# Performance work log

Hardware: AMD Instinct MI355X
Metric: run time of the kernel (lower is better)

Reference implementation:

```python
import jax, jax.numpy as jnp
import numpy as np

D_MODEL = 528
N_HEADS = 16
FEAT = 16           # feature_dim
HEAD_DIM = 33       # d_model // num_heads == 2*FEAT + 1 (required by the module's math)
WINDOW = 64
EPS = 1e-9


def setup_inputs() -> dict:
    key = jax.random.key(0)
    ks = jax.random.split(key, 10)
    B, S = 2, 2048
    hidden_states = jax.random.normal(ks[0], (B, S, D_MODEL), dtype=jnp.float32)
    attention_mask = jnp.ones((B, S), dtype=jnp.int32)
    sc = 0.02
    # weights stored as (in, out); torch Linear applies x @ W.T so this is the transposed weight
    Wq_lin = jax.random.normal(ks[1], (D_MODEL, FEAT * N_HEADS), dtype=jnp.float32) * sc
    Wk_lin = jax.random.normal(ks[2], (D_MODEL, FEAT * N_HEADS), dtype=jnp.float32) * sc
    Wv_lin = jax.random.normal(ks[3], (D_MODEL, HEAD_DIM * N_HEADS), dtype=jnp.float32) * sc
    Wo_lin = jax.random.normal(ks[4], (HEAD_DIM * N_HEADS, D_MODEL), dtype=jnp.float32) * sc
    Wq_win = jax.random.normal(ks[5], (D_MODEL, D_MODEL), dtype=jnp.float32) * sc
    Wk_win = jax.random.normal(ks[6], (D_MODEL, D_MODEL), dtype=jnp.float32) * sc
    Wv_win = jax.random.normal(ks[7], (D_MODEL, D_MODEL), dtype=jnp.float32) * sc
    Wo_win = jax.random.normal(ks[8], (D_MODEL, D_MODEL), dtype=jnp.float32) * sc
    return {
        "hidden_states": hidden_states,
        "attention_mask": attention_mask,
        "Wq_lin": Wq_lin, "Wk_lin": Wk_lin, "Wv_lin": Wv_lin, "Wo_lin": Wo_lin,
        "Wq_win": Wq_win, "Wk_win": Wk_win, "Wv_win": Wv_win, "Wo_win": Wo_win,
    }


def _linear_attention(x, mask, Wq, Wk, Wv, Wo):
    B, S, _ = x.shape
    q = (x @ Wq).reshape(B, S, N_HEADS, FEAT).transpose(0, 2, 1, 3)      # bhsf
    k = (x @ Wk).reshape(B, S, N_HEADS, FEAT).transpose(0, 2, 1, 3)
    v = (x @ Wv).reshape(B, S, N_HEADS, HEAD_DIM).transpose(0, 2, 1, 3)  # bhse
    # Taylor feature map: [1, q, 0.5*q^2] -> feature dim 2*FEAT+1 == HEAD_DIM
    qe = jnp.concatenate([jnp.ones_like(q[..., :1]), q, 0.5 * q * q], axis=-1)
    ke = jnp.concatenate([jnp.ones_like(k[..., :1]), k, 0.5 * k * k], axis=-1)
    kv = jnp.einsum('bhnd,bhne->bhde', ke, v)          # (B,H,Dexp,HEAD_DIM)
    qkv = jnp.einsum('bhnd,bhde->bhne', qe, kv)        # (B,H,S,HEAD_DIM)
    # z[b,h,n,e] = (sum_d qe[b,h,n,d]) * ksum[b,h,e]  (faithful to torch einsum with size-1 n)
    z = qe.sum(-1, keepdims=True) * ke.sum(2, keepdims=True)  # (B,H,S,Dexp==HEAD_DIM)
    out = qkv / (z + EPS)
    out = jnp.where((mask == 0)[:, None, :, None], 0.0, out)
    out = out.transpose(0, 2, 1, 3).reshape(B, S, N_HEADS * HEAD_DIM)
    return out @ Wo


def _window_attention(x, mask, Wq, Wk, Wv, Wo):
    B, S, _ = x.shape
    q = (x @ Wq).reshape(B, S, N_HEADS, HEAD_DIM).transpose(0, 2, 1, 3)
    k = (x @ Wk).reshape(B, S, N_HEADS, HEAD_DIM).transpose(0, 2, 1, 3)
    v = (x @ Wv).reshape(B, S, N_HEADS, HEAD_DIM).transpose(0, 2, 1, 3)
    scores = jnp.einsum('bhnd,bhmd->bhnm', q, k) / np.sqrt(HEAD_DIM).astype(np.float32)
    # tril(diagonal=window_size-1): allow key index m <= n + WINDOW - 1
    i = jnp.arange(S)[:, None]
    j = jnp.arange(S)[None, :]
    band = (j <= i + WINDOW - 1)
    neg_inf = jnp.asarray(-jnp.inf, scores.dtype)
    scores = jnp.where(band[None, None], scores, neg_inf)
    scores = jnp.where((mask == 0)[:, None, None, :], neg_inf, scores)
    attn = jax.nn.softmax(scores, axis=-1)
    out = jnp.einsum('bhnm,bhmd->bhnd', attn, v)
    out = out.transpose(0, 2, 1, 3).reshape(B, S, D_MODEL)
    return out @ Wo


def reference(hidden_states, attention_mask,
              Wq_lin, Wk_lin, Wv_lin, Wo_lin,
              Wq_win, Wk_win, Wv_win, Wo_win):
    lin = _linear_attention(hidden_states, attention_mask, Wq_lin, Wk_lin, Wv_lin, Wo_lin)
    win = _window_attention(hidden_states, attention_mask, Wq_win, Wk_win, Wv_win, Wo_win)
    return lin + win
```

## Files before the change

kernel.cpp:

```cpp
#include <hip/hip_runtime.h>

#define NH 16
#define FEAT 16
#define HD 33
#define DM 528
#define WIN 64
#define EPSF 1e-9f
#define K1C (0.17407765595569785f * 1.4426950408889634f)
#define KP 544
#define KSPLIT 1632
#define NPROJ 2112
#define KOUT 1056
#define OPS 4352
#define NCH 16
#define ZPARTS 4

typedef float f32x4 __attribute__((ext_vector_type(4)));
typedef short short8 __attribute__((ext_vector_type(8)));

__device__ inline ushort f2bf(float f) {
  uint u = __float_as_uint(f);
  uint r = u + 0x7fffu + ((u >> 16) & 1u);
  return (ushort)(r >> 16);
}
__device__ inline ushort f2bf_tr(float f) { return (ushort)(__float_as_uint(f) >> 16); }
__device__ inline float bf2f(ushort u) { return __uint_as_float(((uint)u) << 16); }

__global__ __launch_bounds__(256) void prep_all(const float* __restrict__ x,
                                                const float* __restrict__ Wq_lin,
                                                const float* __restrict__ Wk_lin,
                                                const float* __restrict__ Wv_lin,
                                                const float* __restrict__ Wo_lin,
                                                const float* __restrict__ Wq_win,
                                                const float* __restrict__ Wk_win,
                                                const float* __restrict__ Wv_win,
                                                const float* __restrict__ Wo_win,
                                                ushort* __restrict__ xhi,
                                                ushort* __restrict__ xlo,
                                                ushort* __restrict__ Wqks,
                                                ushort* __restrict__ WprojT,
                                                ushort* __restrict__ WoT2, int M) {
  const int stride = gridDim.x * 256;
  const int tid0 = blockIdx.x * 256 + threadIdx.x;
  for (int j = tid0; j < M * 68; j += stride) {
    int row = j / 68, c8 = (j - row * 68) * 8;
    short8 h8, l8;
    if (c8 < DM) {
      float4 f0 = *(const float4*)&x[(size_t)row * DM + c8];
      float4 f1 = *(const float4*)&x[(size_t)row * DM + c8 + 4];
      float vv[8] = {f0.x, f0.y, f0.z, f0.w, f1.x, f1.y, f1.z, f1.w};
#pragma unroll
      for (int z = 0; z < 8; ++z) {
        ushort h = f2bf(vv[z]);
        h8[z] = (short)h;
        l8[z] = (short)f2bf(vv[z] - bf2f(h));
      }
    } else {
      h8 = (short8){0, 0, 0, 0, 0, 0, 0, 0};
      l8 = h8;
    }
    *(short8*)&xhi[(size_t)row * KP + c8] = h8;
    *(short8*)&xlo[(size_t)row * KP + c8] = l8;
  }
  for (int i = tid0; i < 512 * KSPLIT; i += stride) {
    int n = i / KSPLIT, kp = i - n * KSPLIT;
    int seg = kp / KP, kk = kp - seg * KP;
    float v = 0.f;
    if (kk < DM) v = (n < 256) ? Wq_lin[(size_t)kk * 256 + n] : Wk_lin[(size_t)kk * 256 + (n - 256)];
    ushort h = f2bf(v);
    if (seg == 2) h = f2bf(v - bf2f(h));
    Wqks[i] = h;
  }
  for (int i = tid0; i < NPROJ * KP; i += stride) {
    int n = i / KP, k = i - n * KP;
    float v = 0.f;
    if (k < DM) {
      if (n < DM) v = Wq_win[(size_t)k * DM + n];
      else if (n < 2 * DM) v = Wk_win[(size_t)k * DM + (n - DM)] * K1C;
      else if (n < 3 * DM) v = Wv_win[(size_t)k * DM + (n - 2 * DM)];
      else v = Wv_lin[(size_t)k * DM + (n - 3 * DM)];
    }
    WprojT[i] = f2bf(v);
  }
  for (int i = tid0; i < DM * KOUT; i += stride) {
    int n = i / KOUT, k = i - n * KOUT;
    float v = (k < DM) ? Wo_lin[(size_t)k * DM + n] : Wo_win[(size_t)(k - DM) * DM + n];
    WoT2[i] = f2bf(v);
  }
}

__global__ __launch_bounds__(256) void proj_fused(const ushort* __restrict__ xhi,
                                                  const ushort* __restrict__ xlo,
                                                  const ushort* __restrict__ Wqks,
                                                  const ushort* __restrict__ WprojT,
                                                  float* __restrict__ qk,
                                                  ushort* __restrict__ qkvw,
                                                  float* __restrict__ v_lin,
                                                  const int* __restrict__ maskp,
                                                  int S) {
  __shared__ ushort As[128][36];
  __shared__ ushort Bs[128][36];
  const int bm = blockIdx.x * 128;
  const int tid = threadIdx.x;
  const int lane = tid & 63, w = tid >> 6;
  const int lo = lane & 15, hi = lane >> 4;
  const int wr = w >> 1, wc = w & 1;
  const short8 zv = {0, 0, 0, 0, 0, 0, 0, 0};
  f32x4 acc[4][4];
#pragma unroll
  for (int mb = 0; mb < 4; ++mb)
#pragma unroll
    for (int nb = 0; nb < 4; ++nb) acc[mb][nb] = (f32x4){0.f, 0.f, 0.f, 0.f};

  if (blockIdx.y < 17) {
    const int bn = blockIdx.y * 128;
    for (int k0 = 0; k0 < KP; k0 += 32) {
      short8 a_ld[2], b_ld[2];
#pragma unroll
      for (int p = 0; p < 2; ++p) {
        int c = tid + p * 256;
        int row = c >> 2, cc = c & 3;
        a_ld[p] = *(const short8*)&xhi[(size_t)(bm + row) * KP + k0 + cc * 8];
        int bnr = bn + row;
        b_ld[p] = (bnr < NPROJ) ? *(const short8*)&WprojT[(size_t)bnr * KP + k0 + cc * 8] : zv;
      }
      __syncthreads();
#pragma unroll
      for (int p = 0; p < 2; ++p) {
        int c = tid + p * 256;
        int row = c >> 2, cc = c & 3;
        *(short8*)&As[row][cc * 8] = a_ld[p];
        *(short8*)&Bs[row][cc * 8] = b_ld[p];
      }
      __syncthreads();
      short8 afr[4], bfr[4];
#pragma unroll
      for (int mb = 0; mb < 4; ++mb) afr[mb] = *(const short8*)&As[wr * 64 + 16 * mb + lo][8 * hi];
#pragma unroll
      for (int nb = 0; nb < 4; ++nb) bfr[nb] = *(const short8*)&Bs[wc * 64 + 16 * nb + lo][8 * hi];
#pragma unroll
      for (int mb = 0; mb < 4; ++mb)
#pragma unroll
        for (int nb = 0; nb < 4; ++nb)
          acc[mb][nb] = __builtin_amdgcn_mfma_f32_16x16x32_bf16(afr[mb], bfr[nb], acc[mb][nb], 0, 0, 0);
    }
#pragma unroll
    for (int nb = 0; nb < 4; ++nb) {
      const int col = bn + wc * 64 + 16 * nb + lo;
      if (col >= NPROJ) continue;
      const int seg = col / DM;
      const int cc = col - seg * DM;
      if (seg == 3) {
#pragma unroll
        for (int mb = 0; mb < 4; ++mb)
#pragma unroll
          for (int r = 0; r < 4; ++r) {
            int row = bm + wr * 64 + 16 * mb + 4 * hi + r;
            v_lin[(size_t)row * DM + cc] = acc[mb][nb][r];
          }
      } else {
        const uint h = ((uint)cc * 993u) >> 15;
        const int e = cc - (int)h * 33;
        ushort* dst = qkvw + (size_t)seg * (32u * (uint)S * 40u);
#pragma unroll
        for (int mb = 0; mb < 4; ++mb)
#pragma unroll
          for (int r = 0; r < 4; ++r) {
            int row = bm + wr * 64 + 16 * mb + 4 * hi + r;
            int b = (row >= S) ? 1 : 0;
            int nn = row - b * S;
            float val = acc[mb][nb][r];
            if (seg == 2) {
              size_t tb = (size_t)(b * NH + (int)h) * 40;
              dst[(tb + e) * S + nn] = f2bf(val);
              if (e == 0) {
                dst[(tb + 33) * S + nn] = 0x3F80;
#pragma unroll
                for (int z = 34; z < 40; ++z) dst[(tb + z) * S + nn] = 0;
              }
            } else {
              size_t base = ((size_t)(b * NH + (int)h) * S + nn) * 40;
              dst[base + e] = f2bf(val);
              if (e == 0) {
                ushort pad33 = (seg == 0) ? (ushort)0x3F80
                                          : (maskp[row] ? (ushort)0 : f2bf(-1e30f));
                dst[base + 33] = pad33;
#pragma unroll
                for (int z = 34; z < 40; ++z) dst[base + z] = 0;
              }
            }
          }
      }
    }
  } else {
    const int bn = (blockIdx.y - 17) * 128;
    for (int k0 = 0; k0 < KSPLIT; k0 += 32) {
      const int seg = k0 / KP;
      const int kk = k0 - seg * KP;
      const ushort* xsrc = (seg == 1) ? xlo : xhi;
      short8 a_ld[2], b_ld[2];
#pragma unroll
      for (int p = 0; p < 2; ++p) {
        int c = tid + p * 256;
        int row = c >> 2, cc = c & 3;
        a_ld[p] = *(const short8*)&xsrc[(size_t)(bm + row) * KP + kk + cc * 8];
        b_ld[p] = *(const short8*)&Wqks[(size_t)(bn + row) * KSPLIT + k0 + cc * 8];
      }
      __syncthreads();
#pragma unroll
      for (int p = 0; p < 2; ++p) {
        int c = tid + p * 256;
        int row = c >> 2, cc = c & 3;
        *(short8*)&As[row][cc * 8] = a_ld[p];
        *(short8*)&Bs[row][cc * 8] = b_ld[p];
      }
      __syncthreads();
      short8 afr[4], bfr[4];
#pragma unroll
      for (int mb = 0; mb < 4; ++mb) afr[mb] = *(const short8*)&As[wr * 64 + 16 * mb + lo][8 * hi];
#pragma unroll
      for (int nb = 0; nb < 4; ++nb) bfr[nb] = *(const short8*)&Bs[wc * 64 + 16 * nb + lo][8 * hi];
#pragma unroll
      for (int mb = 0; mb < 4; ++mb)
#pragma unroll
        for (int nb = 0; nb < 4; ++nb)
          acc[mb][nb] = __builtin_amdgcn_mfma_f32_16x16x32_bf16(afr[mb], bfr[nb], acc[mb][nb], 0, 0, 0);
    }
#pragma unroll
    for (int mb = 0; mb < 4; ++mb)
#pragma unroll
      for (int nb = 0; nb < 4; ++nb) {
        int col = bn + wc * 64 + 16 * nb + lo;
#pragma unroll
        for (int r = 0; r < 4; ++r) {
          int row = bm + wr * 64 + 16 * mb + 4 * hi + r;
          qk[(size_t)row * 512 + col] = acc[mb][nb][r];
        }
      }
  }
}

__global__ __launch_bounds__(256) void gemm_out(const ushort* __restrict__ A,
                                                const ushort* __restrict__ Bt,
                                                float* __restrict__ C, int S) {
  __shared__ ushort As[128][36];
  __shared__ ushort Bs[128][36];
  const int bm = blockIdx.x * 128, bn = blockIdx.y * 128;
  const int tid = threadIdx.x;
  const int lane = tid & 63, w = tid >> 6;
  const int lo = lane & 15, hi = lane >> 4;
  const int wr = w >> 1, wc = w & 1;
  f32x4 acc[4][4];
#pragma unroll
  for (int mb = 0; mb < 4; ++mb)
#pragma unroll
    for (int nb = 0; nb < 4; ++nb) acc[mb][nb] = (f32x4){0.f, 0.f, 0.f, 0.f};
  const short8 zv = {0, 0, 0, 0, 0, 0, 0, 0};

  for (int k0 = 0; k0 < KOUT; k0 += 32) {
    short8 a_ld[2], b_ld[2];
#pragma unroll
    for (int p = 0; p < 2; ++p) {
      int c = tid + p * 256;
      int row = c >> 2, cc = c & 3;
      a_ld[p] = *(const short8*)&A[(size_t)(bm + row) * KOUT + k0 + cc * 8];
      int bnr = bn + row;
      b_ld[p] = (bnr < DM) ? *(const short8*)&Bt[(size_t)bnr * KOUT + k0 + cc * 8] : zv;
    }
    __syncthreads();
#pragma unroll
    for (int p = 0; p < 2; ++p) {
      int c = tid + p * 256;
      int row = c >> 2, cc = c & 3;
      *(short8*)&As[row][cc * 8] = a_ld[p];
      *(short8*)&Bs[row][cc * 8] = b_ld[p];
    }
    __syncthreads();
    short8 afr[4], bfr[4];
#pragma unroll
    for (int mb = 0; mb < 4; ++mb) afr[mb] = *(const short8*)&As[wr * 64 + 16 * mb + lo][8 * hi];
#pragma unroll
    for (int nb = 0; nb < 4; ++nb) bfr[nb] = *(const short8*)&Bs[wc * 64 + 16 * nb + lo][8 * hi];
#pragma unroll
    for (int mb = 0; mb < 4; ++mb)
#pragma unroll
      for (int nb = 0; nb < 4; ++nb)
        acc[mb][nb] = __builtin_amdgcn_mfma_f32_16x16x32_bf16(afr[mb], bfr[nb], acc[mb][nb], 0, 0, 0);
  }
#pragma unroll
  for (int nb = 0; nb < 4; ++nb) {
    const int col = bn + wc * 64 + 16 * nb + lo;
    if (col >= DM) continue;
#pragma unroll
    for (int mb = 0; mb < 4; ++mb)
#pragma unroll
      for (int r = 0; r < 4; ++r) {
        int row = bm + wr * 64 + 16 * mb + 4 * hi + r;
        C[(size_t)row * DM + col] = acc[mb][nb][r];
      }
  }
}

__global__ __launch_bounds__(256) void lin_red(const float* __restrict__ kvp,
                                               float* __restrict__ kvr) {
  int bh = blockIdx.x;
  for (int i = threadIdx.x; i < 1188; i += 256) {
    float s = 0.f;
#pragma unroll
    for (int c = 0; c < NCH; ++c) s += kvp[(size_t)(bh * NCH + c) * 1188 + i];
    kvr[(size_t)bh * 1188 + i] = s;
  }
}

__global__ __launch_bounds__(256) void win_kv(const ushort* __restrict__ qwb,
                                              const ushort* __restrict__ kwb,
                                              const ushort* __restrict__ vwbT,
                                              ushort* __restrict__ Opart,
                                              const float* __restrict__ qk,
                                              const float* __restrict__ v_lin,
                                              float* __restrict__ kvp,
                                              int B, int S, int NT2) {
  __shared__ ushort sh[4][32][72];
  const int tid = threadIdx.x;
  const int NWINBLK = NT2 * 32 * ZPARTS;
  const int bx = blockIdx.x;

  if (bx < NWINBLK) {
    const int bh = bx & 31;
    const int qp = bx >> 5;
    const int part = qp / NT2;
    const int qt = NT2 - 1 - (qp - part * NT2);
    const int NT = NT2 * 2;
    const int T = min(NT, 2 * qt + 3);
    if (part >= T) return;
    const int n0 = qt * 128;
    const int lane = tid & 63, w = tid >> 6;
    const int lo = lane & 15, hi = lane >> 4;
    const short8 zv = {0, 0, 0, 0, 0, 0, 0, 0};
    ushort (*Ps)[32][72] = sh;

    short8 qf[2][2];
#pragma unroll
    for (int qr = 0; qr < 2; ++qr) {
      const ushort* qrow = qwb + ((size_t)bh * S + n0 + w * 32 + qr * 16 + lo) * 40;
      qf[qr][0] = *(const short8*)&qrow[8 * hi];
      qf[qr][1] = (hi == 0) ? *(const short8*)&qrow[32] : zv;
    }

    const ushort* kb = kwb + (size_t)bh * S * 40;
    const ushort* vb = vwbT + (size_t)bh * 40 * S;
    int evc[3];
#pragma unroll
    for (int eb = 0; eb < 3; ++eb) {
      int e = 16 * eb + lo;
      evc[eb] = (e > 39) ? 39 : e;
    }

    f32x4 Oacc[2][3];
#pragma unroll
    for (int qr = 0; qr < 2; ++qr)
#pragma unroll
      for (int eb = 0; eb < 3; ++eb) Oacc[qr][eb] = (f32x4){0.f, 0.f, 0.f, 0.f};

    for (int t = part; t < T; t += ZPARTS) {
      const int m0 = t * 64;
      short8 kf0[4], kf1[4];
#pragma unroll
      for (int bb = 0; bb < 4; ++bb) {
        const ushort* kr = kb + (size_t)(m0 + 16 * bb + lo) * 40;
        kf0[bb] = *(const short8*)&kr[8 * hi];
        kf1[bb] = *(const short8*)&kr[32];
      }
      short8 vf0[3], vf1[3];
#pragma unroll
      for (int eb = 0; eb < 3; ++eb) {
        const ushort* vr = vb + (size_t)evc[eb] * S + m0;
        vf0[eb] = *(const short8*)&vr[8 * hi];
        vf1[eb] = *(const short8*)&vr[32 + 8 * hi];
      }

      f32x4 accS[2][4];
#pragma unroll
      for (int qr = 0; qr < 2; ++qr)
#pragma unroll
        for (int bb = 0; bb < 4; ++bb) accS[qr][bb] = (f32x4){0.f, 0.f, 0.f, 0.f};
      __builtin_amdgcn_s_setprio(1);
#pragma unroll
      for (int bb = 0; bb < 4; ++bb)
#pragma unroll
        for (int qr = 0; qr < 2; ++qr) {
          accS[qr][bb] = __builtin_amdgcn_mfma_f32_16x16x32_bf16(qf[qr][0], kf0[bb], accS[qr][bb], 0, 0, 0);
          accS[qr][bb] = __builtin_amdgcn_mfma_f32_16x16x32_bf16(qf[qr][1], kf1[bb], accS[qr][bb], 0, 0, 0);
        }
      __builtin_amdgcn_s_setprio(0);

      const bool boundary = (m0 > n0);
      const int dmn = m0 - n0;
#pragma unroll
      for (int qr = 0; qr < 2; ++qr)
#pragma unroll
        for (int bb = 0; bb < 4; ++bb)
#pragma unroll
          for (int r = 0; r < 4; ++r) {
            float p = exp2f(accS[qr][bb][r]);
            if (boundary) {
              int rr = w * 32 + qr * 16 + 4 * hi + r;
              int c = 16 * bb + lo;
              if (c > rr + 63 - dmn) p = 0.f;
            }
            Ps[w][qr * 16 + 4 * hi + r][16 * bb + lo] = f2bf_tr(p);
          }

      __builtin_amdgcn_s_setprio(1);
#pragma unroll
      for (int qr = 0; qr < 2; ++qr) {
        short8 pf0 = *(const short8*)&Ps[w][qr * 16 + lo][8 * hi];
        short8 pf1 = *(const short8*)&Ps[w][qr * 16 + lo][32 + 8 * hi];
#pragma unroll
        for (int eb = 0; eb < 3; ++eb) {
          Oacc[qr][eb] = __builtin_amdgcn_mfma_f32_16x16x32_bf16(pf0, vf0[eb], Oacc[qr][eb], 0, 0, 0);
          Oacc[qr][eb] = __builtin_amdgcn_mfma_f32_16x16x32_bf16(pf1, vf1[eb], Oacc[qr][eb], 0, 0, 0);
        }
      }
      __builtin_amdgcn_s_setprio(0);
    }

    const size_t ob = ((size_t)(bh * NT2 + qt) * ZPARTS + part) * OPS;
#pragma unroll
    for (int qr = 0; qr < 2; ++qr)
#pragma unroll
      for (int eb = 0; eb < 3; ++eb) {
        int e = 16 * eb + lo;
        if (e < 34) {
#pragma unroll
          for (int r = 0; r < 4; ++r)
            Opart[ob + (size_t)(w * 32 + qr * 16 + 4 * hi + r) * 34 + e] = f2bf(Oacc[qr][eb][r]);
        }
      }
  } else {
    const int idx = bx - NWINBLK;
    const int bh = idx & 31, chunk = idx >> 5;
    const int b = bh >> 4, h = bh & 15;
    float* kraw = (float*)sh;
    float* vsh = kraw + 64 * 17;
    if (tid < 64) { vsh[tid * 36 + 33] = 1.f; vsh[tid * 36 + 34] = 0.f; vsh[tid * 36 + 35] = 0.f; }
    f32x4 acc0 = {0.f, 0.f, 0.f, 0.f}, acc1 = {0.f, 0.f, 0.f, 0.f};
    const int d0 = tid / 9, c40 = (tid % 9) * 4;
    const int idx1 = tid + 256;
    const int d1 = idx1 / 9, c41 = (idx1 % 9) * 4;
    const int SC = S / NCH;
    const int nbeg = chunk * SC;
    __syncthreads();
    for (int n0 = nbeg; n0 < nbeg + SC; n0 += 64) {
      {
        int row = tid >> 2, f4 = (tid & 3) * 4;
        float4 kv4 = *(const float4*)&qk[(size_t)(b * S + n0 + row) * 512 + 256 + h * 16 + f4];
        kraw[row * 17 + f4 + 0] = kv4.x; kraw[row * 17 + f4 + 1] = kv4.y;
        kraw[row * 17 + f4 + 2] = kv4.z; kraw[row * 17 + f4 + 3] = kv4.w;
      }
      for (int i = tid; i < 64 * 33; i += 256) {
        int n = i / 33, e = i - n * 33;
        vsh[n * 36 + e] = v_lin[(size_t)(b * S + n0 + n) * DM + h * HD + e];
      }
      __syncthreads();
#pragma unroll 4
      for (int n = 0; n < 64; ++n) {
        {
          float ke;
          if (d0 == 0) ke = 1.f;
          else if (d0 < 17) ke = kraw[n * 17 + d0 - 1];
          else { float kk = kraw[n * 17 + d0 - 17]; ke = 0.5f * kk * kk; }
          f32x4 v = *(const f32x4*)&vsh[n * 36 + c40];
          acc0 += ke * v;
        }
        if (idx1 < 297) {
          float ke;
          if (d1 < 17) ke = kraw[n * 17 + d1 - 1];
          else { float kk = kraw[n * 17 + d1 - 17]; ke = 0.5f * kk * kk; }
          f32x4 v = *(const f32x4*)&vsh[n * 36 + c41];
          acc1 += ke * v;
        }
      }
      __syncthreads();
    }
    float* dst = kvp + (size_t)(bh * NCH + chunk) * 1188;
    *(f32x4*)&dst[d0 * 36 + c40] = acc0;
    if (idx1 < 297) *(f32x4*)&dst[d1 * 36 + c41] = acc1;
  }
}

__global__ __launch_bounds__(256) void comb_lin(const ushort* __restrict__ Opart,
                                                const float* __restrict__ qk,
                                                const float* __restrict__ kvr,
                                                const int* __restrict__ mask,
                                                ushort* __restrict__ cat,
                                                int B, int S, int NT2) {
  __shared__ float shf[160];
  const int tid = threadIdx.x;
  const int NCOMB = NT2 * 32;
  const int bx = blockIdx.x;

  if (bx < NCOMB) {
    const int bh = bx & 31;
    const int qt = bx >> 5;
    const int b = bh >> 4, h = bh & 15;
    const int T = min(NT2 * 2, 2 * qt + 3);
    const int P = min(ZPARTS, T);
    const size_t base = (size_t)(bh * NT2 + qt) * ZPARTS * OPS;
    float* linv = shf;
    if (tid < 128) {
      float l = 0.f;
      for (int p = 0; p < P; ++p) l += bf2f(Opart[base + (size_t)p * OPS + tid * 34 + 33]);
      linv[tid] = (l > 0.f) ? 1.f / l : 0.f;
    }
    __syncthreads();
    for (int i = tid; i < 128 * 33; i += 256) {
      int row = i / 33, e = i - row * 33;
      float o = 0.f;
      for (int p = 0; p < P; ++p) o += bf2f(Opart[base + (size_t)p * OPS + row * 34 + e]);
      int n = qt * 128 + row;
      cat[((size_t)(b * S + n)) * KOUT + DM + h * HD + e] = f2bf(o * linv[row]);
    }
  } else {
    const int bs = bx - NCOMB;
    const int b = (bs >= S) ? 1 : 0;
    float* qsh = shf;
    __shared__ float qsh2[NH * 17];
    qsh = qsh2;
    for (int i = tid; i < NH * FEAT; i += 256)
      qsh[(i >> 4) * 17 + (i & 15)] = qk[(size_t)bs * 512 + i];
    __syncthreads();
    const int msk = mask[bs];
    for (int o = tid; o < DM; o += 256) {
      uint h = ((uint)o * 993u) >> 15;
      int e = o - (int)h * 33;
      const float* kvh = kvr + (size_t)(b * NH + (int)h) * 1188;
      float qsum = 1.f, qkv = kvh[e];
#pragma unroll
      for (int f = 0; f < FEAT; ++f) {
        float q = qsh[h * 17 + f];
        float q2 = 0.5f * q * q;
        qsum += q + q2;
        qkv += q * kvh[(1 + f) * 36 + e] + q2 * kvh[(17 + f) * 36 + e];
      }
      float z = qsum * kvh[e * 36 + 33];
      float outv = qkv / (z + EPSF);
      if (msk == 0) outv = 0.f;
      cat[(size_t)bs * KOUT + o] = f2bf(outv);
    }
  }
}

extern "C" void kernel_launch(void* const* d_in, const int* in_sizes, int n_in,
                              void* d_out, int out_size, void* d_ws, size_t ws_size,
                              hipStream_t stream) {
  const float* x      = (const float*)d_in[0];
  const int*   mask   = (const int*)d_in[1];
  const float* Wq_lin = (const float*)d_in[2];
  const float* Wk_lin = (const float*)d_in[3];
  const float* Wv_lin = (const float*)d_in[4];
  const float* Wo_lin = (const float*)d_in[5];
  const float* Wq_win = (const float*)d_in[6];
  const float* Wk_win = (const float*)d_in[7];
  const float* Wv_win = (const float*)d_in[8];
  const float* Wo_win = (const float*)d_in[9];
  float* out = (float*)d_out;

  const int BS = in_sizes[1];
  const int B = 2;
  const int S = BS / B;
  const int NT2 = S / 128;
  const int M = BS;

  float* ws = (float*)d_ws;
  float* qk      = ws;  ws += (size_t)BS * 512;
  float* v_lin   = ws;  ws += (size_t)BS * DM;
  float* kvp     = ws;  ws += (size_t)B * NH * NCH * 1188;
  float* kvr     = ws;  ws += (size_t)B * NH * 1188;
  ushort* ub     = (ushort*)ws;
  ushort* x_hi   = ub;  ub += (size_t)M * KP;
  ushort* x_lo   = ub;  ub += (size_t)M * KP;
  ushort* qkvw   = ub;  ub += (size_t)3 * 32 * S * 40;
  ushort* cat    = ub;  ub += (size_t)M * KOUT;
  ushort* WprojT = ub;  ub += (size_t)NPROJ * KP;
  ushort* WoT2   = ub;  ub += (size_t)DM * KOUT;
  ushort* Wqks   = ub;  ub += (size_t)512 * KSPLIT;
  ushort* Opart  = ub;  ub += (size_t)32 * NT2 * ZPARTS * OPS;

  ushort* qwb  = qkvw;
  ushort* kwb  = qkvw + (size_t)32 * S * 40;
  ushort* vwbT = qkvw + (size_t)64 * S * 40;

  dim3 blk(256);

  prep_all<<<2048, blk, 0, stream>>>(x, Wq_lin, Wk_lin, Wv_lin, Wo_lin,
                                     Wq_win, Wk_win, Wv_win, Wo_win,
                                     x_hi, x_lo, Wqks, WprojT, WoT2, M);

  proj_fused<<<dim3(M / 128, 21), blk, 0, stream>>>(x_hi, x_lo, Wqks, WprojT,
                                                    qk, qkvw, v_lin, mask, S);

  win_kv<<<dim3(NT2 * 32 * ZPARTS + B * NH * NCH), blk, 0, stream>>>(
      qwb, kwb, vwbT, Opart, qk, v_lin, kvp, B, S, NT2);

  lin_red<<<dim3(B * NH), blk, 0, stream>>>(kvp, kvr);

  comb_lin<<<dim3(NT2 * 32 + BS), blk, 0, stream>>>(Opart, qk, kvr, mask, cat, B, S, NT2);

  gemm_out<<<dim3(M / 128, (DM + 127) / 128), blk, 0, stream>>>(cat, WoT2, out, S);
}
```

Before: 193.1 us.

## Split-K the qk projection with atomics, persistent work queue, smaller gemm_out tiles

The qk projection's three-segment K loop is split across separate blocks that accumulate into a zeroed qk buffer with atomicAdd, which raises the block count. win_kv becomes a persistent kernel that pulls window and linear-kv work items from eight atomic counters, replacing the fixed grid mapping. gemm_out moves to 64-row tiles so more blocks run. The changes trade extra atomic traffic, a qk zeroing pass and queue overhead for better load balance and occupancy, and atomic accumulation makes the summation order nondeterministic.

```diff
diff --git a/kernel.cpp b/kernel.cpp
--- a/kernel.cpp
+++ b/kernel.cpp
@@ -39,9 +39,12 @@
                                                 ushort* __restrict__ xlo,
                                                 ushort* __restrict__ Wqks,
                                                 ushort* __restrict__ WprojT,
-                                                ushort* __restrict__ WoT2, int M) {
+                                                ushort* __restrict__ WoT2,
+                                                float* __restrict__ qk,
+                                                int* __restrict__ ctr, int M) {
   const int stride = gridDim.x * 256;
   const int tid0 = blockIdx.x * 256 + threadIdx.x;
+  if (tid0 < 8) ctr[tid0] = 0;
   for (int j = tid0; j < M * 68; j += stride) {
     int row = j / 68, c8 = (j - row * 68) * 8;
     short8 h8, l8;
@@ -62,6 +65,8 @@
     *(short8*)&xhi[(size_t)row * KP + c8] = h8;
     *(short8*)&xlo[(size_t)row * KP + c8] = l8;
   }
+  for (int i = tid0; i < M * 128; i += stride)
+    ((float4*)qk)[i] = make_float4(0.f, 0.f, 0.f, 0.f);
   for (int i = tid0; i < 512 * KSPLIT; i += stride) {
     int n = i / KSPLIT, kp = i - n * KSPLIT;
     int seg = kp / KP, kk = kp - seg * KP;
@@ -193,18 +198,19 @@
       }
     }
   } else {
-    const int bn = (blockIdx.y - 17) * 128;
-    for (int k0 = 0; k0 < KSPLIT; k0 += 32) {
-      const int seg = k0 / KP;
-      const int kk = k0 - seg * KP;
-      const ushort* xsrc = (seg == 1) ? xlo : xhi;
+    const int yy = blockIdx.y - 17;
+    const int seg = yy >> 2;
+    const int bn = (yy & 3) * 128;
+    const ushort* xsrc = (seg == 1) ? xlo : xhi;
+    const int kb = seg * KP;
+    for (int k0 = 0; k0 < KP; k0 += 32) {
       short8 a_ld[2], b_ld[2];
 #pragma unroll
       for (int p = 0; p < 2; ++p) {
         int c = tid + p * 256;
         int row = c >> 2, cc = c & 3;
-        a_ld[p] = *(const short8*)&xsrc[(size_t)(bm + row) * KP + kk + cc * 8];
-        b_ld[p] = *(const short8*)&Wqks[(size_t)(bn + row) * KSPLIT + k0 + cc * 8];
+        a_ld[p] = *(const short8*)&xsrc[(size_t)(bm + row) * KP + k0 + cc * 8];
+        b_ld[p] = *(const short8*)&Wqks[(size_t)(bn + row) * KSPLIT + kb + k0 + cc * 8];
       }
       __syncthreads();
 #pragma unroll
@@ -234,7 +240,7 @@
 #pragma unroll
         for (int r = 0; r < 4; ++r) {
           int row = bm + wr * 64 + 16 * mb + 4 * hi + r;
-          qk[(size_t)row * 512 + col] = acc[mb][nb][r];
+          atomicAdd(&qk[(size_t)row * 512 + col], acc[mb][nb][r]);
         }
       }
   }
@@ -243,46 +249,52 @@
 __global__ __launch_bounds__(256) void gemm_out(const ushort* __restrict__ A,
                                                 const ushort* __restrict__ Bt,
                                                 float* __restrict__ C, int S) {
-  __shared__ ushort As[128][36];
+  __shared__ ushort As[64][36];
   __shared__ ushort Bs[128][36];
-  const int bm = blockIdx.x * 128, bn = blockIdx.y * 128;
+  const int bm = blockIdx.x * 64, bn = blockIdx.y * 128;
   const int tid = threadIdx.x;
   const int lane = tid & 63, w = tid >> 6;
   const int lo = lane & 15, hi = lane >> 4;
-  const int wr = w >> 1, wc = w & 1;
-  f32x4 acc[4][4];
-#pragma unroll
-  for (int mb = 0; mb < 4; ++mb)
+  const int wr = w & 1, wc = w >> 1;
+  f32x4 acc[2][4];
+#pragma unroll
+  for (int mb = 0; mb < 2; ++mb)
 #pragma unroll
     for (int nb = 0; nb < 4; ++nb) acc[mb][nb] = (f32x4){0.f, 0.f, 0.f, 0.f};
   const short8 zv = {0, 0, 0, 0, 0, 0, 0, 0};
 
   for (int k0 = 0; k0 < KOUT; k0 += 32) {
-    short8 a_ld[2], b_ld[2];
+    short8 a_ld, b_ld[2];
+    {
+      int row = tid >> 2, cc = tid & 3;
+      a_ld = *(const short8*)&A[(size_t)(bm + row) * KOUT + k0 + cc * 8];
+    }
 #pragma unroll
     for (int p = 0; p < 2; ++p) {
       int c = tid + p * 256;
       int row = c >> 2, cc = c & 3;
-      a_ld[p] = *(const short8*)&A[(size_t)(bm + row) * KOUT + k0 + cc * 8];
       int bnr = bn + row;
       b_ld[p] = (bnr < DM) ? *(const short8*)&Bt[(size_t)bnr * KOUT + k0 + cc * 8] : zv;
     }
     __syncthreads();
+    {
+      int row = tid >> 2, cc = tid & 3;
+      *(short8*)&As[row][cc * 8] = a_ld;
+    }
 #pragma unroll
     for (int p = 0; p < 2; ++p) {
       int c = tid + p * 256;
       int row = c >> 2, cc = c & 3;
-      *(short8*)&As[row][cc * 8] = a_ld[p];
       *(short8*)&Bs[row][cc * 8] = b_ld[p];
     }
     __syncthreads();
-    short8 afr[4], bfr[4];
-#pragma unroll
-    for (int mb = 0; mb < 4; ++mb) afr[mb] = *(const short8*)&As[wr * 64 + 16 * mb + lo][8 * hi];
+    short8 afr[2], bfr[4];
+#pragma unroll
+    for (int mb = 0; mb < 2; ++mb) afr[mb] = *(const short8*)&As[wr * 32 + 16 * mb + lo][8 * hi];
 #pragma unroll
     for (int nb = 0; nb < 4; ++nb) bfr[nb] = *(const short8*)&Bs[wc * 64 + 16 * nb + lo][8 * hi];
 #pragma unroll
-    for (int mb = 0; mb < 4; ++mb)
+    for (int mb = 0; mb < 2; ++mb)
 #pragma unroll
       for (int nb = 0; nb < 4; ++nb)
         acc[mb][nb] = __builtin_amdgcn_mfma_f32_16x16x32_bf16(afr[mb], bfr[nb], acc[mb][nb], 0, 0, 0);
@@ -292,10 +304,10 @@
     const int col = bn + wc * 64 + 16 * nb + lo;
     if (col >= DM) continue;
 #pragma unroll
-    for (int mb = 0; mb < 4; ++mb)
+    for (int mb = 0; mb < 2; ++mb)
 #pragma unroll
       for (int r = 0; r < 4; ++r) {
-        int row = bm + wr * 64 + 16 * mb + 4 * hi + r;
+        int row = bm + wr * 32 + 16 * mb + 4 * hi + r;
         C[(size_t)row * DM + col] = acc[mb][nb][r];
       }
   }
@@ -319,173 +331,195 @@
                                               const float* __restrict__ qk,
                                               const float* __restrict__ v_lin,
                                               float* __restrict__ kvp,
+                                              int* __restrict__ ctr,
                                               int B, int S, int NT2) {
   __shared__ ushort sh[4][32][72];
+  __shared__ int s_item;
   const int tid = threadIdx.x;
-  const int NWINBLK = NT2 * 32 * ZPARTS;
-  const int bx = blockIdx.x;
-
-  if (bx < NWINBLK) {
-    const int bh = bx & 31;
-    const int qp = bx >> 5;
-    const int part = qp / NT2;
-    const int qt = NT2 - 1 - (qp - part * NT2);
-    const int NT = NT2 * 2;
-    const int T = min(NT, 2 * qt + 3);
-    if (part >= T) return;
-    const int n0 = qt * 128;
-    const int lane = tid & 63, w = tid >> 6;
-    const int lo = lane & 15, hi = lane >> 4;
-    const short8 zv = {0, 0, 0, 0, 0, 0, 0, 0};
-    ushort (*Ps)[32][72] = sh;
-
-    short8 qf[2][2];
-#pragma unroll
-    for (int qr = 0; qr < 2; ++qr) {
-      const ushort* qrow = qwb + ((size_t)bh * S + n0 + w * 32 + qr * 16 + lo) * 40;
-      qf[qr][0] = *(const short8*)&qrow[8 * hi];
-      qf[qr][1] = (hi == 0) ? *(const short8*)&qrow[32] : zv;
-    }
-
-    const ushort* kb = kwb + (size_t)bh * S * 40;
-    const ushort* vb = vwbT + (size_t)bh * 40 * S;
-    int evc[3];
-#pragma unroll
-    for (int eb = 0; eb < 3; ++eb) {
-      int e = 16 * eb + lo;
-      evc[eb] = (e > 39) ? 39 : e;
-    }
-
-    f32x4 Oacc[2][3];
-#pragma unroll
-    for (int qr = 0; qr < 2; ++qr)
-#pragma unroll
-      for (int eb = 0; eb < 3; ++eb) Oacc[qr][eb] = (f32x4){0.f, 0.f, 0.f, 0.f};
-
-    for (int t = part; t < T; t += ZPARTS) {
-      const int m0 = t * 64;
-      short8 kf0[4], kf1[4];
-#pragma unroll
-      for (int bb = 0; bb < 4; ++bb) {
-        const ushort* kr = kb + (size_t)(m0 + 16 * bb + lo) * 40;
-        kf0[bb] = *(const short8*)&kr[8 * hi];
-        kf1[bb] = *(const short8*)&kr[32];
-      }
-      short8 vf0[3], vf1[3];
-#pragma unroll
-      for (int eb = 0; eb < 3; ++eb) {
-        const ushort* vr = vb + (size_t)evc[eb] * S + m0;
-        vf0[eb] = *(const short8*)&vr[8 * hi];
-        vf1[eb] = *(const short8*)&vr[32 + 8 * hi];
-      }
-
-      f32x4 accS[2][4];
-#pragma unroll
-      for (int qr = 0; qr < 2; ++qr)
-#pragma unroll
-        for (int bb = 0; bb < 4; ++bb) accS[qr][bb] = (f32x4){0.f, 0.f, 0.f, 0.f};
-      __builtin_amdgcn_s_setprio(1);
-#pragma unroll
-      for (int bb = 0; bb < 4; ++bb)
-#pragma unroll
-        for (int qr = 0; qr < 2; ++qr) {
-          accS[qr][bb] = __builtin_amdgcn_mfma_f32_16x16x32_bf16(qf[qr][0], kf0[bb], accS[qr][bb], 0, 0, 0);
-          accS[qr][bb] = __builtin_amdgcn_mfma_f32_16x16x32_bf16(qf[qr][1], kf1[bb], accS[qr][bb], 0, 0, 0);
-        }
-      __builtin_amdgcn_s_setprio(0);
-
-      const bool boundary = (m0 > n0);
-      const int dmn = m0 - n0;
-#pragma unroll
-      for (int qr = 0; qr < 2; ++qr)
-#pragma unroll
-        for (int bb = 0; bb < 4; ++bb)
-#pragma unroll
-          for (int r = 0; r < 4; ++r) {
-            float p = exp2f(accS[qr][bb][r]);
-            if (boundary) {
-              int rr = w * 32 + qr * 16 + 4 * hi + r;
-              int c = 16 * bb + lo;
-              if (c > rr + 63 - dmn) p = 0.f;
-            }
-            Ps[w][qr * 16 + 4 * hi + r][16 * bb + lo] = f2bf_tr(p);
-          }
-
-      __builtin_amdgcn_s_setprio(1);
+  const int qid = blockIdx.x & 7;
+  const int WINQ = NT2 * 16;
+  const int QTOT = WINQ + 4 * NCH;
+
+  for (;;) {
+    __syncthreads();
+    if (tid == 0) {
+      int item = -1;
+      for (int a = 0; a < 8; ++a) {
+        int q = (qid + a) & 7;
+        int wi = atomicAdd(&ctr[q], 1);
+        if (wi < QTOT) { item = q * QTOT + wi; break; }
+      }
+      s_item = item;
+    }
+    __syncthreads();
+    const int it = s_item;
+    if (it < 0) return;
+    const int q = it / QTOT;
+    const int wi = it - q * QTOT;
+
+    if (wi < WINQ) {
+      const int qt = NT2 - 1 - (wi >> 4);
+      const int sub = wi & 15;
+      const int part = sub >> 2;
+      const int bh = q + 8 * (sub & 3);
+      const int NT = NT2 * 2;
+      const int T = min(NT, 2 * qt + 3);
+      if (part >= T) continue;
+      const int n0 = qt * 128;
+      const int lane = tid & 63, w = tid >> 6;
+      const int lo = lane & 15, hi = lane >> 4;
+      const short8 zv = {0, 0, 0, 0, 0, 0, 0, 0};
+      ushort (*Ps)[32][72] = sh;
+
+      short8 qf[2][2];
 #pragma unroll
       for (int qr = 0; qr < 2; ++qr) {
-        short8 pf0 = *(const short8*)&Ps[w][qr * 16 + lo][8 * hi];
-        short8 pf1 = *(const short8*)&Ps[w][qr * 16 + lo][32 + 8 * hi];
-#pragma unroll
-        for (int eb = 0; eb < 3; ++eb) {
-          Oacc[qr][eb] = __builtin_amdgcn_mfma_f32_16x16x32_bf16(pf0, vf0[eb], Oacc[qr][eb], 0, 0, 0);
-          Oacc[qr][eb] = __builtin_amdgcn_mfma_f32_16x16x32_bf16(pf1, vf1[eb], Oacc[qr][eb], 0, 0, 0);
-        }
-      }
-      __builtin_amdgcn_s_setprio(0);
-    }
-
-    const size_t ob = ((size_t)(bh * NT2 + qt) * ZPARTS + part) * OPS;
-#pragma unroll
-    for (int qr = 0; qr < 2; ++qr)
+        const ushort* qrow = qwb + ((size_t)bh * S + n0 + w * 32 + qr * 16 + lo) * 40;
+        qf[qr][0] = *(const short8*)&qrow[8 * hi];
+        qf[qr][1] = (hi == 0) ? *(const short8*)&qrow[32] : zv;
+      }
+
+      const ushort* kb = kwb + (size_t)bh * S * 40;
+      const ushort* vb = vwbT + (size_t)bh * 40 * S;
+      int evc[3];
 #pragma unroll
       for (int eb = 0; eb < 3; ++eb) {
         int e = 16 * eb + lo;
-        if (e < 34) {
-#pragma unroll
-          for (int r = 0; r < 4; ++r)
-            Opart[ob + (size_t)(w * 32 + qr * 16 + 4 * hi + r) * 34 + e] = f2bf(Oacc[qr][eb][r]);
-        }
-      }
-  } else {
-    const int idx = bx - NWINBLK;
-    const int bh = idx & 31, chunk = idx >> 5;
-    const int b = bh >> 4, h = bh & 15;
-    float* kraw = (float*)sh;
-    float* vsh = kraw + 64 * 17;
-    if (tid < 64) { vsh[tid * 36 + 33] = 1.f; vsh[tid * 36 + 34] = 0.f; vsh[tid * 36 + 35] = 0.f; }
-    f32x4 acc0 = {0.f, 0.f, 0.f, 0.f}, acc1 = {0.f, 0.f, 0.f, 0.f};
-    const int d0 = tid / 9, c40 = (tid % 9) * 4;
-    const int idx1 = tid + 256;
-    const int d1 = idx1 / 9, c41 = (idx1 % 9) * 4;
-    const int SC = S / NCH;
-    const int nbeg = chunk * SC;
-    __syncthreads();
-    for (int n0 = nbeg; n0 < nbeg + SC; n0 += 64) {
-      {
-        int row = tid >> 2, f4 = (tid & 3) * 4;
-        float4 kv4 = *(const float4*)&qk[(size_t)(b * S + n0 + row) * 512 + 256 + h * 16 + f4];
-        kraw[row * 17 + f4 + 0] = kv4.x; kraw[row * 17 + f4 + 1] = kv4.y;
-        kraw[row * 17 + f4 + 2] = kv4.z; kraw[row * 17 + f4 + 3] = kv4.w;
-      }
-      for (int i = tid; i < 64 * 33; i += 256) {
-        int n = i / 33, e = i - n * 33;
-        vsh[n * 36 + e] = v_lin[(size_t)(b * S + n0 + n) * DM + h * HD + e];
-      }
+        evc[eb] = (e > 39) ? 39 : e;
+      }
+
+      f32x4 Oacc[2][3];
+#pragma unroll
+      for (int qr = 0; qr < 2; ++qr)
+#pragma unroll
+        for (int eb = 0; eb < 3; ++eb) Oacc[qr][eb] = (f32x4){0.f, 0.f, 0.f, 0.f};
+
+      for (int t = part; t < T; t += ZPARTS) {
+        const int m0 = t * 64;
+        short8 kf0[4], kf1[4];
+#pragma unroll
+        for (int bb = 0; bb < 4; ++bb) {
+          const ushort* kr = kb + (size_t)(m0 + 16 * bb + lo) * 40;
+          kf0[bb] = *(const short8*)&kr[8 * hi];
+          kf1[bb] = *(const short8*)&kr[32];
+        }
+        short8 vf0[3], vf1[3];
+#pragma unroll
+        for (int eb = 0; eb < 3; ++eb) {
+          const ushort* vr = vb + (size_t)evc[eb] * S + m0;
+          vf0[eb] = *(const short8*)&vr[8 * hi];
+          vf1[eb] = *(const short8*)&vr[32 + 8 * hi];
+        }
+
+        f32x4 accS[2][4];
+#pragma unroll
+        for (int qr = 0; qr < 2; ++qr)
+#pragma unroll
+          for (int bb = 0; bb < 4; ++bb) accS[qr][bb] = (f32x4){0.f, 0.f, 0.f, 0.f};
+        __builtin_amdgcn_s_setprio(1);
+#pragma unroll
+        for (int bb = 0; bb < 4; ++bb)
+#pragma unroll
+          for (int qr = 0; qr < 2; ++qr) {
+            accS[qr][bb] = __builtin_amdgcn_mfma_f32_16x16x32_bf16(qf[qr][0], kf0[bb], accS[qr][bb], 0, 0, 0);
+            accS[qr][bb] = __builtin_amdgcn_mfma_f32_16x16x32_bf16(qf[qr][1], kf1[bb], accS[qr][bb], 0, 0, 0);
+          }
+        __builtin_amdgcn_s_setprio(0);
+
+        const bool boundary = (m0 > n0);
+        const int dmn = m0 - n0;
+#pragma unroll
+        for (int qr = 0; qr < 2; ++qr)
+#pragma unroll
+          for (int bb = 0; bb < 4; ++bb)
+#pragma unroll
+            for (int r = 0; r < 4; ++r) {
+              float p = exp2f(accS[qr][bb][r]);
+              if (boundary) {
+                int rr = w * 32 + qr * 16 + 4 * hi + r;
+                int c = 16 * bb + lo;
+                if (c > rr + 63 - dmn) p = 0.f;
+              }
+              Ps[w][qr * 16 + 4 * hi + r][16 * bb + lo] = f2bf_tr(p);
+            }
+
+        __builtin_amdgcn_s_setprio(1);
+#pragma unroll
+        for (int qr = 0; qr < 2; ++qr) {
+          short8 pf0 = *(const short8*)&Ps[w][qr * 16 + lo][8 * hi];
+          short8 pf1 = *(const short8*)&Ps[w][qr * 16 + lo][32 + 8 * hi];
+#pragma unroll
+          for (int eb = 0; eb < 3; ++eb) {
+            Oacc[qr][eb] = __builtin_amdgcn_mfma_f32_16x16x32_bf16(pf0, vf0[eb], Oacc[qr][eb], 0, 0, 0);
+            Oacc[qr][eb] = __builtin_amdgcn_mfma_f32_16x16x32_bf16(pf1, vf1[eb], Oacc[qr][eb], 0, 0, 0);
+          }
+        }
+        __builtin_amdgcn_s_setprio(0);
+      }
+
+      const size_t ob = ((size_t)(bh * NT2 + qt) * ZPARTS + part) * OPS;
+#pragma unroll
+      for (int qr = 0; qr < 2; ++qr)
+#pragma unroll
+        for (int eb = 0; eb < 3; ++eb) {
+          int e = 16 * eb + lo;
+          if (e < 34) {
+#pragma unroll
+            for (int r = 0; r < 4; ++r)
+              Opart[ob + (size_t)(w * 32 + qr * 16 + 4 * hi + r) * 34 + e] = f2bf(Oacc[qr][eb][r]);
+          }
+        }
+    } else {
+      const int j = wi - WINQ;
+      const int bh = q + 8 * (j & 3);
+      const int chunk = j >> 2;
+      const int b = bh >> 4, h = bh & 15;
+      float* kraw = (float*)sh;
+      float* vsh = kraw + 64 * 17;
+      if (tid < 64) { vsh[tid * 36 + 33] = 1.f; vsh[tid * 36 + 34] = 0.f; vsh[tid * 36 + 35] = 0.f; }
+      f32x4 acc0 = {0.f, 0.f, 0.f, 0.f}, acc1 = {0.f, 0.f, 0.f, 0.f};
+      const int d0 = tid / 9, c40 = (tid % 9) * 4;
+      const int idx1 = tid + 256;
+      const int d1 = idx1 / 9, c41 = (idx1 % 9) * 4;
+      const int SC = S / NCH;
+      const int nbeg = chunk * SC;
       __syncthreads();
+      for (int n0 = nbeg; n0 < nbeg + SC; n0 += 64) {
+        {
+          int row = tid >> 2, f4 = (tid & 3) * 4;
+          float4 kv4 = *(const float4*)&qk[(size_t)(b * S + n0 + row) * 512 + 256 + h * 16 + f4];
+          kraw[row * 17 + f4 + 0] = kv4.x; kraw[row * 17 + f4 + 1] = kv4.y;
+          kraw[row * 17 + f4 + 2] = kv4.z; kraw[row * 17 + f4 + 3] = kv4.w;
+        }
+        for (int i = tid; i < 64 * 33; i += 256) {
+          int n = i / 33, e = i - n * 33;
+          vsh[n * 36 + e] = v_lin[(size_t)(b * S + n0 + n) * DM + h * HD + e];
+        }
+        __syncthreads();
 #pragma unroll 4
-      for (int n = 0; n < 64; ++n) {
-        {
-          float ke;
-          if (d0 == 0) ke = 1.f;
-          else if (d0 < 17) ke = kraw[n * 17 + d0 - 1];
-          else { float kk = kraw[n * 17 + d0 - 17]; ke = 0.5f * kk * kk; }
-          f32x4 v = *(const f32x4*)&vsh[n * 36 + c40];
-          acc0 += ke * v;
-        }
-        if (idx1 < 297) {
-          float ke;
-          if (d1 < 17) ke = kraw[n * 17 + d1 - 1];
-          else { float kk = kraw[n * 17 + d1 - 17]; ke = 0.5f * kk * kk; }
-          f32x4 v = *(const f32x4*)&vsh[n * 36 + c41];
-          acc1 += ke * v;
-        }
-      }
-      __syncthreads();
-    }
-    float* dst = kvp + (size_t)(bh * NCH + chunk) * 1188;
-    *(f32x4*)&dst[d0 * 36 + c40] = acc0;
-    if (idx1 < 297) *(f32x4*)&dst[d1 * 36 + c41] = acc1;
+        for (int n = 0; n < 64; ++n) {
+          {
+            float ke;
+            if (d0 == 0) ke = 1.f;
+            else if (d0 < 17) ke = kraw[n * 17 + d0 - 1];
+            else { float kk = kraw[n * 17 + d0 - 17]; ke = 0.5f * kk * kk; }
+            f32x4 v = *(const f32x4*)&vsh[n * 36 + c40];
+            acc0 += ke * v;
+          }
+          if (idx1 < 297) {
+            float ke;
+            if (d1 < 17) ke = kraw[n * 17 + d1 - 1];
+            else { float kk = kraw[n * 17 + d1 - 17]; ke = 0.5f * kk * kk; }
+            f32x4 v = *(const f32x4*)&vsh[n * 36 + c41];
+            acc1 += ke * v;
+          }
+        }
+        __syncthreads();
+      }
+      float* dst = kvp + (size_t)(bh * NCH + chunk) * 1188;
+      *(f32x4*)&dst[d0 * 36 + c40] = acc0;
+      if (idx1 < 297) *(f32x4*)&dst[d1 * 36 + c41] = acc1;
+    }
   }
 }
 
@@ -524,9 +558,8 @@
   } else {
     const int bs = bx - NCOMB;
     const int b = (bs >= S) ? 1 : 0;
-    float* qsh = shf;
     __shared__ float qsh2[NH * 17];
-    qsh = qsh2;
+    float* qsh = qsh2;
     for (int i = tid; i < NH * FEAT; i += 256)
       qsh[(i >> 4) * 17 + (i & 15)] = qk[(size_t)bs * 512 + i];
     __syncthreads();
@@ -573,6 +606,7 @@
   const int M = BS;
 
   float* ws = (float*)d_ws;
+  int* ctr       = (int*)ws;  ws += 8;
   float* qk      = ws;  ws += (size_t)BS * 512;
   float* v_lin   = ws;  ws += (size_t)BS * DM;
   float* kvp     = ws;  ws += (size_t)B * NH * NCH * 1188;
@@ -595,17 +629,17 @@
 
   prep_all<<<2048, blk, 0, stream>>>(x, Wq_lin, Wk_lin, Wv_lin, Wo_lin,
                                      Wq_win, Wk_win, Wv_win, Wo_win,
-                                     x_hi, x_lo, Wqks, WprojT, WoT2, M);
-
-  proj_fused<<<dim3(M / 128, 21), blk, 0, stream>>>(x_hi, x_lo, Wqks, WprojT,
+                                     x_hi, x_lo, Wqks, WprojT, WoT2, qk, ctr, M);
+
+  proj_fused<<<dim3(M / 128, 29), blk, 0, stream>>>(x_hi, x_lo, Wqks, WprojT,
                                                     qk, qkvw, v_lin, mask, S);
 
-  win_kv<<<dim3(NT2 * 32 * ZPARTS + B * NH * NCH), blk, 0, stream>>>(
-      qwb, kwb, vwbT, Opart, qk, v_lin, kvp, B, S, NT2);
+  win_kv<<<dim3(1536), blk, 0, stream>>>(qwb, kwb, vwbT, Opart, qk, v_lin, kvp,
+                                         ctr, B, S, NT2);
 
   lin_red<<<dim3(B * NH), blk, 0, stream>>>(kvp, kvr);
 
   comb_lin<<<dim3(NT2 * 32 + BS), blk, 0, stream>>>(Opart, qk, kvr, mask, cat, B, S, NT2);
 
-  gemm_out<<<dim3(M / 128, (DM + 127) / 128), blk, 0, stream>>>(cat, WoT2, out, S);
-}
+  gemm_out<<<dim3(M / 64, (DM + 127) / 128), blk, 0, stream>>>(cat, WoT2, out, S);
+}
```

Result: slower. 356.6 us (+84.7%).
